# Performance work log

Hardware: AMD Instinct MI355X
Metric: run time of the kernel (lower is better)

## Reference

```python
import jax, jax.numpy as jnp
import numpy as np

N, IN, H, C, E = 50000, 128, 2, 64, 800000
HC = H * C  # 128
NEG_SLOPE = 0.2
EPS_GN = 1e-5


def setup_inputs() -> dict:
    key = jax.random.key(0)
    ks = jax.random.split(key, 32)
    r = lambda i, shape: jax.random.normal(ks[i], shape, dtype=jnp.float32) * 0.1
    inp = {
        'x': jax.random.normal(ks[0], (N, IN), dtype=jnp.float32),
        'edge_index': jax.random.randint(ks[1], (2, E), 0, N, dtype=jnp.int64),
        # conv 0: in=128 -> heads*emb=128
        'Wl0': r(2, (IN, HC)), 'bl0': jnp.zeros((HC,), jnp.float32),
        'Wr0': r(3, (IN, HC)), 'br0': jnp.zeros((HC,), jnp.float32),
        'att0': r(4, (H, C)), 'bias0': jnp.zeros((HC,), jnp.float32),
        # conv 1: in=128 -> 128
        'Wl1': r(5, (HC, HC)), 'bl1': jnp.zeros((HC,), jnp.float32),
        'Wr1': r(6, (HC, HC)), 'br1': jnp.zeros((HC,), jnp.float32),
        'att1': r(7, (H, C)), 'bias1': jnp.zeros((HC,), jnp.float32),
        # GraphNorm params (weight, bias, mean_scale)
        'g0': jnp.ones((HC,), jnp.float32), 'be0': jnp.zeros((HC,), jnp.float32), 'ms0': jnp.ones((HC,), jnp.float32),
        'g1': jnp.ones((HC,), jnp.float32), 'be1': jnp.zeros((HC,), jnp.float32), 'ms1': jnp.ones((HC,), jnp.float32),
        # MLP head
        'W1': r(8, (HC, C)), 'b1': jnp.zeros((C,), jnp.float32),
        'W2': r(9, (C, 2)), 'b2': jnp.zeros((2,), jnp.float32),
    }
    return inp


def gatv2_conv(x, src, dst, Wl, bl, Wr, br, att, bias):
    # PyG GATv2Conv: separate source/target transforms, edge attention, segment softmax
    xl = (x @ Wl + bl).reshape(N, H, C)  # source features
    xr = (x @ Wr + br).reshape(N, H, C)  # target features
    m = jax.nn.leaky_relu(xl[src] + xr[dst], NEG_SLOPE)  # [Etot, H, C]
    e = jnp.einsum('ehc,hc->eh', m, att)                  # [Etot, H]
    emax = jax.ops.segment_max(e, dst, num_segments=N)    # stable softmax per dst
    ex = jnp.exp(e - emax[dst])
    denom = jax.ops.segment_sum(ex, dst, num_segments=N)
    alpha = ex / (denom[dst] + 1e-16)
    out = jax.ops.segment_sum(xl[src] * alpha[:, :, None], dst, num_segments=N)
    return out.reshape(N, HC) + bias


def graph_norm(x, gamma, beta, mean_scale):
    # PyG GraphNorm with batch=None (single graph)
    mean = x.mean(axis=0)
    out = x - mean_scale * mean
    var = (out * out).mean(axis=0)
    return gamma * out / jnp.sqrt(var + EPS_GN) + beta


def reference(x, edge_index, Wl0, bl0, Wr0, br0, att0, bias0,
              Wl1, bl1, Wr1, br1, att1, bias1,
              g0, be0, ms0, g1, be1, ms1, W1, b1, W2, b2):
    loop = jnp.arange(N, dtype=edge_index.dtype)
    src = jnp.concatenate([edge_index[0], loop])  # add_self_loops=True
    dst = jnp.concatenate([edge_index[1], loop])
    # layer 0 (conv + GraphNorm + ReLU)
    h = jax.nn.relu(graph_norm(gatv2_conv(x, src, dst, Wl0, bl0, Wr0, br0, att0, bias0), g0, be0, ms0))
    # layer 1
    h = jax.nn.relu(graph_norm(gatv2_conv(h, src, dst, Wl1, bl1, Wr1, br1, att1, bias1), g1, be1, ms1))
    # dropout is identity in eval mode
    h = jax.nn.relu(h @ W1 + b1)
    return h @ W2 + b2
```

## Files before the change

kernel.cpp:

```cpp
#include <hip/hip_runtime.h>
#include <hip/hip_bf16.h>

#define N_NODES 50000
#define NE      800000
#define NETOT   (NE + N_NODES)
#define NEG     0.2f
#define NBUCK   196
#define NSEG    64
#define SEGCAP  128
#define NCTR    (NBUCK * NSEG)
#define NSLOT   256

typedef unsigned short u16;
typedef unsigned int   u32;
typedef __attribute__((ext_vector_type(8))) short bf16x8;
typedef __attribute__((ext_vector_type(4))) float f32x4;

__device__ __forceinline__ float b2f(u16 v) {
    union { float f; u32 u; } c; c.u = ((u32)v) << 16; return c.f;
}
__device__ __forceinline__ u16 f2b(float f) {
    union { float f; u32 u; } c; c.f = f;
    u32 r = c.u + 0x7FFF + ((c.u >> 16) & 1);
    return (u16)(r >> 16);
}
__device__ __forceinline__ float ldf(const void* p, int i, int fmt) {
    return fmt ? b2f(((const u16*)p)[i]) : ((const float*)p)[i];
}

__device__ __forceinline__ float red16(float p) {
    union { float f; int i; } a, b;
    a.f = p; b.i = __builtin_amdgcn_update_dpp(0, a.i, 0xB1,  0xF, 0xF, true); p += b.f;
    a.f = p; b.i = __builtin_amdgcn_update_dpp(0, a.i, 0x4E,  0xF, 0xF, true); p += b.f;
    a.f = p; b.i = __builtin_amdgcn_update_dpp(0, a.i, 0x141, 0xF, 0xF, true); p += b.f;
    a.f = p; b.i = __builtin_amdgcn_update_dpp(0, a.i, 0x140, 0xF, 0xF, true); p += b.f;
    return p;
}

__device__ __forceinline__ float lrelu(float v) {
    return fmaf(0.4f, fabsf(v), 0.6f * v);
}

__global__ void init_all(const u32* __restrict__ xw, const u32* __restrict__ w0,
                         const int* __restrict__ ei,
                         int* __restrict__ flag, int* __restrict__ bcnt,
                         float* __restrict__ Sp1, float* __restrict__ Sp2) {
    int g = blockIdx.x * 256 + threadIdx.x;
    if (g < NCTR) bcnt[g] = 0;
    for (int i = g; i < NSLOT * 128; i += gridDim.x * 256) {
        Sp1[i] = 0.f; Sp2[i] = 0.f;
    }
    if (blockIdx.x == 0) {
        int wv = threadIdx.x >> 6, l = threadIdx.x & 63;
        if (wv == 0) {
            u32 v = xw[l * 50000 + 1];
            u32 e = (v >> 7) & 0xFF;
            unsigned long long m = __ballot(e >= 100 && e <= 140);
            if (l == 0) { flag[0] = (__popcll(m) >= 48) ? 1 : 0; flag[1] = 0; }
        } else if (wv == 1) {
            u32 v = w0[l * 128 + 1];
            u32 e = (v >> 7) & 0xFF;
            unsigned long long m = __ballot(e >= 100 && e <= 140);
            if (l == 0) flag[3] = (__popcll(m) >= 48) ? 1 : 0;
        } else if (wv == 2) {
            int v = ei[(l * 25000) | 1];
            unsigned long long nz = __ballot(v != 0);
            if (l == 0) flag[2] = (nz == 0ULL) ? 1 : 0;
        }
    }
}

__global__ void bin_a(const int* __restrict__ ei, const int* __restrict__ flag,
                      int* __restrict__ bcnt, u32* __restrict__ pairs) {
    int e = blockIdx.x * 256 + threadIdx.x;
    if (e >= NE) return;
    int f = flag[2];
    int s, d;
    if (f) { s = ei[2 * e]; d = ei[2 * (NE + e)]; }
    else   { s = ei[e];     d = ei[NE + e]; }
    int idx = (d >> 8) * NSEG + (blockIdx.x & (NSEG - 1));
    int pos = atomicAdd(&bcnt[idx], 1);
    if (pos < SEGCAP)
        pairs[(size_t)idx * SEGCAP + pos] = ((u32)(d & 255) << 16) | (u32)s;
}

__global__ __launch_bounds__(256) void bin_b(const u32* __restrict__ pairs,
        const int* __restrict__ bcnt,
        int* __restrict__ indptr, int* __restrict__ srcs) {
    __shared__ int cnt[256];
    __shared__ int scn[256];
    __shared__ int msh[NSEG];
    __shared__ int baseSh;
    int b = blockIdx.x, tid = threadIdx.x;
    int nb0 = b << 8;
    int nodesHere = min(256, N_NODES - nb0);
    if (tid < NSEG) msh[tid] = min(bcnt[b * NSEG + tid], SEGCAP);
    int pre = 0;
    for (int i = tid; i < b * NSEG; i += 256) pre += min(bcnt[i], SEGCAP);
    scn[tid] = pre; __syncthreads();
    for (int off = 128; off > 0; off >>= 1) {
        if (tid < off) scn[tid] += scn[tid + off];
        __syncthreads();
    }
    if (tid == 0) baseSh = scn[0] + nb0;
    __syncthreads();
    int base = baseSh;
    cnt[tid] = (tid < nodesHere) ? 1 : 0;
    __syncthreads();
    const u32* bp = pairs + (size_t)b * NSEG * SEGCAP;
    for (int t = tid; t < NSEG * SEGCAP; t += 256) {
        int seg = t >> 7, i = t & (SEGCAP - 1);
        if (i < msh[seg]) {
            int dloc = (int)(bp[t] >> 16);
            atomicAdd(&cnt[dloc], 1);
        }
    }
    __syncthreads();
    int v = cnt[tid];
    scn[tid] = v; __syncthreads();
    for (int off = 1; off < 256; off <<= 1) {
        int u = (tid >= off) ? scn[tid - off] : 0;
        __syncthreads();
        scn[tid] += u;
        __syncthreads();
    }
    int myoff = base + scn[tid] - v;
    if (tid < nodesHere) indptr[nb0 + tid] = myoff;
    if (tid == 255 && b == NBUCK - 1) indptr[N_NODES] = base + scn[255];
    __syncthreads();
    cnt[tid] = myoff;
    __syncthreads();
    if (tid < nodesHere) {
        int pos = atomicAdd(&cnt[tid], 1);
        srcs[pos] = nb0 + tid;
    }
    for (int t = tid; t < NSEG * SEGCAP; t += 256) {
        int seg = t >> 7, i = t & (SEGCAP - 1);
        if (i < msh[seg]) {
            u32 p = bp[t];
            int pos = atomicAdd(&cnt[p >> 16], 1);
            srcs[pos] = (int)(p & 0xffff);
        }
    }
}

#define LDP 136
#define NT  128
__global__ __launch_bounds__(256) void gemm_xf(const void* __restrict__ inp,
        const int* __restrict__ fin, const int* __restrict__ fw,
        const void* __restrict__ Wl, const void* __restrict__ bl,
        const void* __restrict__ Wr, const void* __restrict__ br,
        const float* __restrict__ nscale, const float* __restrict__ nshift,
        u16* __restrict__ XL, u16* __restrict__ XR) {
    __shared__ u16 As16[NT * LDP];
    __shared__ u16 Bs16[128 * LDP];
    __shared__ float Sc[128], Sh[128];
    int fi = fin[0], fb = fw[0];
    int by = blockIdx.y;
    const void* W  = by ? Wr : Wl;
    const void* bi = by ? br : bl;
    u16* dst       = by ? XR : XL;
    int n0 = blockIdx.x * NT;
    int tid = threadIdx.x;
    bool donorm = (nscale != nullptr);
    if (donorm) {
        if (tid < 128) { Sc[tid] = nscale[tid]; Sh[tid] = nshift[tid]; }
        __syncthreads();
    }
    if (fi) {
        for (int t = tid; t < NT * 16; t += 256) {
            int node = t >> 4, c8 = (t & 15) << 3;
            int n = n0 + node;
            bf16x8 v = {0,0,0,0,0,0,0,0};
            if (n < N_NODES) v = *(const bf16x8*)((const u16*)inp + (size_t)n * 128 + c8);
            *(bf16x8*)&As16[node * LDP + c8] = v;
        }
    } else {
        for (int t = tid; t < NT * 32; t += 256) {
            int node = t >> 5, c4 = (t & 31) << 2;
            int n = n0 + node;
            float4 v = {0.f, 0.f, 0.f, 0.f};
            if (n < N_NODES) v = *(const float4*)((const float*)inp + (size_t)n * 128 + c4);
            if (donorm) {
                v.x = fmaxf(v.x * Sc[c4]     + Sh[c4],     0.f);
                v.y = fmaxf(v.y * Sc[c4 + 1] + Sh[c4 + 1], 0.f);
                v.z = fmaxf(v.z * Sc[c4 + 2] + Sh[c4 + 2], 0.f);
                v.w = fmaxf(v.w * Sc[c4 + 3] + Sh[c4 + 3], 0.f);
            }
            ushort4 h;
            h.x = f2b(v.x); h.y = f2b(v.y); h.z = f2b(v.z); h.w = f2b(v.w);
            *(ushort4*)&As16[node * LDP + c4] = h;
        }
    }
    if (fb) {
        for (int t = tid; t < 128 * 16; t += 256) {
            int k = t >> 4, j8 = (t & 15) << 3;
            bf16x8 v = *(const bf16x8*)((const u16*)W + k * 128 + j8);
            #pragma unroll
            for (int q = 0; q < 8; ++q) Bs16[(j8 + q) * LDP + k] = (u16)v[q];
        }
    } else {
        for (int t = tid; t < 128 * 32; t += 256) {
            int k = t >> 5, j4 = (t & 31) << 2;
            float4 v = *(const float4*)((const float*)W + k * 128 + j4);
            Bs16[(j4 + 0) * LDP + k] = f2b(v.x);
            Bs16[(j4 + 1) * LDP + k] = f2b(v.y);
            Bs16[(j4 + 2) * LDP + k] = f2b(v.z);
            Bs16[(j4 + 3) * LDP + k] = f2b(v.w);
        }
    }
    __syncthreads();

    int wv = tid >> 6, lane = tid & 63;
    int quad = lane >> 4, r = lane & 15;
    int m0 = wv * 32;
    f32x4 acc[2][8];
    #pragma unroll
    for (int mt = 0; mt < 2; ++mt)
        #pragma unroll
        for (int jt = 0; jt < 8; ++jt) acc[mt][jt] = (f32x4){0.f, 0.f, 0.f, 0.f};
    #pragma unroll
    for (int ks = 0; ks < 4; ++ks) {
        int ko = ks * 32 + quad * 8;
        bf16x8 af0 = *(const bf16x8*)&As16[(m0 + r) * LDP + ko];
        bf16x8 af1 = *(const bf16x8*)&As16[(m0 + 16 + r) * LDP + ko];
        #pragma unroll
        for (int jt = 0; jt < 8; ++jt) {
            bf16x8 bfr = *(const bf16x8*)&Bs16[(jt * 16 + r) * LDP + ko];
            acc[0][jt] = __builtin_amdgcn_mfma_f32_16x16x32_bf16(af0, bfr, acc[0][jt], 0, 0, 0);
            acc[1][jt] = __builtin_amdgcn_mfma_f32_16x16x32_bf16(af1, bfr, acc[1][jt], 0, 0, 0);
        }
    }
    __syncthreads();
    #pragma unroll
    for (int jt = 0; jt < 8; ++jt) {
        int j = jt * 16 + r;
        float bj = ldf(bi, j, fb);
        #pragma unroll
        for (int mt = 0; mt < 2; ++mt) {
            #pragma unroll
            for (int reg = 0; reg < 4; ++reg) {
                As16[(m0 + mt * 16 + quad * 4 + reg) * LDP + j] = f2b(acc[mt][jt][reg] + bj);
            }
        }
    }
    __syncthreads();
    #pragma unroll
    for (int rep = 0; rep < 8; ++rep) {
        int idx = rep * 256 + tid;
        int node = idx >> 4, c8 = (idx & 15) << 3;
        int n = n0 + node;
        if (n < N_NODES) {
            bf16x8 v = *(const bf16x8*)&As16[node * LDP + c8];
            *(bf16x8*)(dst + (size_t)n * 128 + c8) = v;
        }
    }
}

__global__ __launch_bounds__(256) void agg_kernel(const u16* __restrict__ XL,
        const u16* __restrict__ XR, const void* __restrict__ att,
        const void* __restrict__ bias,
        const int* __restrict__ fmt,
        const int* __restrict__ indptr, const int* __restrict__ srcs,
        float4* __restrict__ OUT4,
        float* __restrict__ Sp1, float* __restrict__ Sp2) {
    __shared__ float shS1[4 * 128];
    __shared__ float shS2[4 * 128];
    __shared__ int lcount;
    int tid = threadIdx.x;
    int lane = tid & 63;
    int wv = tid >> 6;
    if (tid == 0) lcount = 0;
    __syncthreads();
    int n = blockIdx.x * 4 + wv;
    int eh = lane >> 5, q = lane & 31;
    int fb = fmt[0];
    ushort4 xrv = *(const ushort4*)(XR + (size_t)n * 128 + q * 4);
    float xr0 = b2f(xrv.x), xr1 = b2f(xrv.y), xr2 = b2f(xrv.z), xr3 = b2f(xrv.w);
    float a0 = ldf(att, 4 * q,     fb);
    float a1 = ldf(att, 4 * q + 1, fb);
    float a2 = ldf(att, 4 * q + 2, fb);
    float a3 = ldf(att, 4 * q + 3, fb);
    int beg = indptr[n], end = indptr[n + 1];
    float acc0 = 0.f, acc1 = 0.f, acc2 = 0.f, acc3 = 0.f, dsum = 0.f;
    int nit = (end - beg + 5) / 6;
    for (int it = 0; it < nit; ++it) {
        int iA = beg + 6 * it + eh;
        int iB = iA + 2;
        int iC = iA + 4;
        bool vA = (iA < end), vB = (iB < end), vC = (iC < end);
        int sA = vA ? srcs[iA] : 0;
        int sB = vB ? srcs[iB] : 0;
        int sC = vC ? srcs[iC] : 0;
        ushort4 xa = *(const ushort4*)(XL + (size_t)sA * 128 + q * 4);
        ushort4 xb = *(const ushort4*)(XL + (size_t)sB * 128 + q * 4);
        ushort4 xc = *(const ushort4*)(XL + (size_t)sC * 128 + q * 4);
        float A0 = b2f(xa.x), A1 = b2f(xa.y), A2 = b2f(xa.z), A3 = b2f(xa.w);
        float B0 = b2f(xb.x), B1 = b2f(xb.y), B2v = b2f(xb.z), B3 = b2f(xb.w);
        float C0 = b2f(xc.x), C1 = b2f(xc.y), C2 = b2f(xc.z), C3 = b2f(xc.w);
        float pA = lrelu(A0 + xr0) * a0;
        pA = fmaf(lrelu(A1 + xr1), a1, pA);
        pA = fmaf(lrelu(A2 + xr2), a2, pA);
        pA = fmaf(lrelu(A3 + xr3), a3, pA);
        float pB = lrelu(B0 + xr0) * a0;
        pB = fmaf(lrelu(B1 + xr1), a1, pB);
        pB = fmaf(lrelu(B2v + xr2), a2, pB);
        pB = fmaf(lrelu(B3 + xr3), a3, pB);
        float pC = lrelu(C0 + xr0) * a0;
        pC = fmaf(lrelu(C1 + xr1), a1, pC);
        pC = fmaf(lrelu(C2 + xr2), a2, pC);
        pC = fmaf(lrelu(C3 + xr3), a3, pC);
        pA = red16(pA);
        pB = red16(pB);
        pC = red16(pC);
        float wA = vA ? __expf(fminf(pA, 60.f)) : 0.f;
        float wB = vB ? __expf(fminf(pB, 60.f)) : 0.f;
        float wC = vC ? __expf(fminf(pC, 60.f)) : 0.f;
        acc0 = fmaf(wA, A0, acc0); acc1 = fmaf(wA, A1, acc1);
        acc2 = fmaf(wA, A2, acc2); acc3 = fmaf(wA, A3, acc3);
        acc0 = fmaf(wB, B0, acc0); acc1 = fmaf(wB, B1, acc1);
        acc2 = fmaf(wB, B2v, acc2); acc3 = fmaf(wB, B3, acc3);
        acc0 = fmaf(wC, C0, acc0); acc1 = fmaf(wC, C1, acc1);
        acc2 = fmaf(wC, C2, acc2); acc3 = fmaf(wC, C3, acc3);
        dsum += wA + wB + wC;
    }
    acc0 += __shfl_xor(acc0, 32);
    acc1 += __shfl_xor(acc1, 32);
    acc2 += __shfl_xor(acc2, 32);
    acc3 += __shfl_xor(acc3, 32);
    dsum += __shfl_xor(dsum, 32);
    if (eh == 0) {
        float inv = 1.f / (dsum + 1e-16f);
        float4 o; o.x = acc0 * inv; o.y = acc1 * inv; o.z = acc2 * inv; o.w = acc3 * inv;
        OUT4[(size_t)n * 32 + q] = o;
        float t0 = o.x + ldf(bias, 4 * q,     fb);
        float t1 = o.y + ldf(bias, 4 * q + 1, fb);
        float t2 = o.z + ldf(bias, 4 * q + 2, fb);
        float t3 = o.w + ldf(bias, 4 * q + 3, fb);
        float4 s1; s1.x = t0; s1.y = t1; s1.z = t2; s1.w = t3;
        float4 s2; s2.x = t0 * t0; s2.y = t1 * t1; s2.z = t2 * t2; s2.w = t3 * t3;
        *(float4*)&shS1[wv * 128 + q * 4] = s1;
        *(float4*)&shS2[wv * 128 + q * 4] = s2;
    }
    __threadfence_block();
    int old = 0;
    if (lane == 0) old = atomicAdd(&lcount, 1);
    old = __shfl(old, 0);
    if (old == 3) {
        __threadfence_block();
        int c0 = lane;
        int c1 = lane + 64;
        float s1a = shS1[c0] + shS1[128 + c0] + shS1[256 + c0] + shS1[384 + c0];
        float s1b = shS1[c1] + shS1[128 + c1] + shS1[256 + c1] + shS1[384 + c1];
        float s2a = shS2[c0] + shS2[128 + c0] + shS2[256 + c0] + shS2[384 + c0];
        float s2b = shS2[c1] + shS2[128 + c1] + shS2[256 + c1] + shS2[384 + c1];
        int slot = blockIdx.x & (NSLOT - 1);
        atomicAdd(&Sp1[slot * 128 + c0], s1a);
        atomicAdd(&Sp1[slot * 128 + c1], s1b);
        atomicAdd(&Sp2[slot * 128 + c0], s2a);
        atomicAdd(&Sp2[slot * 128 + c1], s2b);
    }
}

__global__ __launch_bounds__(256) void finalize_norm(float* __restrict__ Sp1,
        float* __restrict__ Sp2,
        const void* __restrict__ gamma, const void* __restrict__ beta,
        const void* __restrict__ msc, const void* __restrict__ bias,
        const int* __restrict__ fmt,
        float* __restrict__ scaleA, float* __restrict__ shiftB) {
    __shared__ float sh1[256], sh2[256];
    int c = blockIdx.x, tid = threadIdx.x;
    sh1[tid] = Sp1[tid * 128 + c];
    sh2[tid] = Sp2[tid * 128 + c];
    Sp1[tid * 128 + c] = 0.f;
    Sp2[tid * 128 + c] = 0.f;
    __syncthreads();
    for (int off = 128; off > 0; off >>= 1) {
        if (tid < off) { sh1[tid] += sh1[tid + off]; sh2[tid] += sh2[tid + off]; }
        __syncthreads();
    }
    if (tid == 0) {
        int fb = fmt[0];
        const float invN = 1.f / (float)N_NODES;
        float mean = sh1[0] * invN;
        float ex2  = sh2[0] * invN;
        float ms = ldf(msc, c, fb);
        float var = ex2 - 2.f * ms * mean * mean + ms * ms * mean * mean;
        float rstd = rsqrtf(var + 1e-5f);
        float A = ldf(gamma, c, fb) * rstd;
        scaleA[c] = A;
        shiftB[c] = ldf(beta, c, fb) - A * (ms * mean - ldf(bias, c, fb));
    }
}

__global__ __launch_bounds__(256) void mlp_kernel(const float* __restrict__ H,
        const void* __restrict__ w1, const void* __restrict__ b1,
        const void* __restrict__ w2, const void* __restrict__ b2,
        const float* __restrict__ nscale, const float* __restrict__ nshift,
        const int* __restrict__ fmt,
        float* __restrict__ out) {
    __shared__ float W1s[128 * 64];
    __shared__ float W2s[128];
    __shared__ float b1s[64];
    __shared__ float Sc[128], Sh[128];
    int tid = threadIdx.x;
    int fb = fmt[0];
    if (fb) {
        for (int t = tid; t < 128 * 8; t += 256) {
            int row8 = t << 3;
            bf16x8 v = *(const bf16x8*)((const u16*)w1 + row8);
            #pragma unroll
            for (int q = 0; q < 8; ++q) W1s[row8 + q] = b2f((u16)v[q]);
        }
    } else {
        for (int t = tid; t < 128 * 64; t += 256) W1s[t] = ((const float*)w1)[t];
    }
    if (tid < 128) { W2s[tid] = ldf(w2, tid, fb); Sc[tid] = nscale[tid]; Sh[tid] = nshift[tid]; }
    if (tid < 64)  b1s[tid] = ldf(b1, tid, fb);
    __syncthreads();
    int n = blockIdx.x * 256 + tid;
    if (n >= N_NODES) return;
    float z[64];
    #pragma unroll
    for (int j = 0; j < 64; j++) z[j] = b1s[j];
    for (int kb = 0; kb < 128; kb += 16) {
        float h[16];
        #pragma unroll
        for (int t = 0; t < 4; t++) {
            float4 v = *(const float4*)&H[n * 128 + kb + t * 4];
            int c = kb + t * 4;
            h[4 * t]     = fmaxf(v.x * Sc[c]     + Sh[c],     0.f);
            h[4 * t + 1] = fmaxf(v.y * Sc[c + 1] + Sh[c + 1], 0.f);
            h[4 * t + 2] = fmaxf(v.z * Sc[c + 2] + Sh[c + 2], 0.f);
            h[4 * t + 3] = fmaxf(v.w * Sc[c + 3] + Sh[c + 3], 0.f);
        }
        #pragma unroll
        for (int i = 0; i < 16; i++) {
            float hv = h[i];
            const float* wrow = &W1s[(kb + i) * 64];
            #pragma unroll
            for (int j = 0; j < 64; j += 4) {
                const float4 w = *(const float4*)&wrow[j];
                z[j]     += hv * w.x;
                z[j + 1] += hv * w.y;
                z[j + 2] += hv * w.z;
                z[j + 3] += hv * w.w;
            }
        }
    }
    float o0 = ldf(b2, 0, fb), o1 = ldf(b2, 1, fb);
    #pragma unroll
    for (int j = 0; j < 64; j++) {
        float zr = fmaxf(z[j], 0.f);
        o0 += zr * W2s[j * 2];
        o1 += zr * W2s[j * 2 + 1];
    }
    if (o0 != o0) o0 = 12345.f;
    if (o1 != o1) o1 = 12345.f;
    float2 o; o.x = o0; o.y = o1;
    ((float2*)out)[n] = o;
}

extern "C" void kernel_launch(void* const* d_in, const int* in_sizes, int n_in,
                              void* d_out, int out_size, void* d_ws, size_t ws_size,
                              hipStream_t stream) {
    (void)in_sizes; (void)n_in; (void)out_size; (void)ws_size;
    const void* x    = d_in[0];
    const int*  ei   = (const int*)d_in[1];
    const void* Wl0  = d_in[2];
    const void* bl0  = d_in[3];
    const void* Wr0  = d_in[4];
    const void* br0  = d_in[5];
    const void* att0 = d_in[6];
    const void* bias0= d_in[7];
    const void* Wl1  = d_in[8];
    const void* bl1  = d_in[9];
    const void* Wr1  = d_in[10];
    const void* br1  = d_in[11];
    const void* att1 = d_in[12];
    const void* bias1= d_in[13];
    const void* g0   = d_in[14];
    const void* be0  = d_in[15];
    const void* ms0  = d_in[16];
    const void* g1   = d_in[17];
    const void* be1  = d_in[18];
    const void* ms1  = d_in[19];
    const void* W1   = d_in[20];
    const void* b1   = d_in[21];
    const void* W2   = d_in[22];
    const void* b2   = d_in[23];

    char* ws = (char*)d_ws;
    const size_t NF2 = (size_t)N_NODES * 128 * 2;
    const size_t NF4 = (size_t)N_NODES * 128 * 4;
    u16*   XLb = (u16*)(ws);
    u16*   XRb = (u16*)(ws + NF2);
    float* B2  = (float*)(ws + 2 * NF2);
    u32*   pairs = (u32*)B2;
    char* small = ws + 2 * NF2 + NF4;
    float* scaleA = (float*)(small + 1024);
    float* shiftB = (float*)(small + 1536);
    int*   flag   = (int*)(small + 2048);
    float* Sp1    = (float*)(small + 4096);
    float* Sp2    = (float*)(small + 4096 + 131072);
    int*   bcnt   = (int*)(small + 4096 + 262144);
    int*   indptr = (int*)(small + 4096 + 262144 + 50176);
    int*   srcs   = indptr + (N_NODES + 64);

    const int* fX   = &flag[0];
    const int* fFP  = &flag[1];
    const int* fPar = &flag[3];

    init_all<<<(NCTR + 255) / 256, 256, 0, stream>>>((const u32*)x, (const u32*)Wl0,
                                                     ei, flag, bcnt, Sp1, Sp2);
    bin_a<<<(NE + 255) / 256, 256, 0, stream>>>(ei, flag, bcnt, pairs);
    bin_b<<<NBUCK, 256, 0, stream>>>(pairs, bcnt, indptr, srcs);

    dim3 ggemm((N_NODES + NT - 1) / NT, 2);

    for (int layer = 0; layer < 2; ++layer) {
        const void* Wl = layer ? Wl1 : Wl0;  const void* bl = layer ? bl1 : bl0;
        const void* Wr = layer ? Wr1 : Wr0;  const void* br = layer ? br1 : br0;
        const void* at = layer ? att1 : att0;
        const void* bi = layer ? bias1 : bias0;
        const void* gm = layer ? g1 : g0;    const void* bt = layer ? be1 : be0;
        const void* mS = layer ? ms1 : ms0;
        const void* inp = layer ? (const void*)B2 : x;
        const int* fin  = layer ? fFP : fX;
        const float* ns = layer ? scaleA : nullptr;
        const float* nh = layer ? shiftB : nullptr;

        gemm_xf<<<ggemm, 256, 0, stream>>>(inp, fin, fPar, Wl, bl, Wr, br, ns, nh,
                                           XLb, XRb);
        agg_kernel<<<(N_NODES + 3) / 4, 256, 0, stream>>>(XLb, XRb, at, bi, fPar,
                                               indptr, srcs, (float4*)B2, Sp1, Sp2);
        finalize_norm<<<128, 256, 0, stream>>>(Sp1, Sp2, gm, bt, mS, bi, fPar,
                                               scaleA, shiftB);
    }

    mlp_kernel<<<(N_NODES + 255) / 256, 256, 0, stream>>>(B2, W1, b1, W2, b2,
                                                          scaleA, shiftB, fPar,
                                                          (float*)d_out);
}
```

Measured before the change: 409.8 us.

## Fuse GraphNorm finalize into aggregation kernel via last-block-done counter

Removes the separate finalize_norm launch per layer. The last aggregation block to finish, detected with a global atomic counter after a threadfence, reduces the per-slot partial sums and writes the norm scale and shift. The slot count drops from 256 to 64 so that final serial reduction stays short. The cost is more atomic contention on fewer slots and a serial tail of work in one wave at the end of the kernel.

```diff
diff --git a/kernel.cpp b/kernel.cpp
--- a/kernel.cpp
+++ b/kernel.cpp
@@ -9,7 +9,8 @@
 #define NSEG    64
 #define SEGCAP  128
 #define NCTR    (NBUCK * NSEG)
-#define NSLOT   256
+#define NSLOT   64
+#define NBLK_AGG ((N_NODES + 3) / 4)
 
 typedef unsigned short u16;
 typedef unsigned int   u32;
@@ -44,12 +45,12 @@
 __global__ void init_all(const u32* __restrict__ xw, const u32* __restrict__ w0,
                          const int* __restrict__ ei,
                          int* __restrict__ flag, int* __restrict__ bcnt,
-                         float* __restrict__ Sp1, float* __restrict__ Sp2) {
+                         float* __restrict__ Sp1, float* __restrict__ Sp2,
+                         int* __restrict__ dctr) {
     int g = blockIdx.x * 256 + threadIdx.x;
     if (g < NCTR) bcnt[g] = 0;
-    for (int i = g; i < NSLOT * 128; i += gridDim.x * 256) {
-        Sp1[i] = 0.f; Sp2[i] = 0.f;
-    }
+    if (g < NSLOT * 128) { Sp1[g] = 0.f; Sp2[g] = 0.f; }
+    if (g == 0) { dctr[0] = 0; dctr[1] = 0; }
     if (blockIdx.x == 0) {
         int wv = threadIdx.x >> 6, l = threadIdx.x & 63;
         if (wv == 0) {
@@ -260,10 +261,14 @@
 __global__ __launch_bounds__(256) void agg_kernel(const u16* __restrict__ XL,
         const u16* __restrict__ XR, const void* __restrict__ att,
         const void* __restrict__ bias,
+        const void* __restrict__ gamma, const void* __restrict__ beta,
+        const void* __restrict__ msc,
         const int* __restrict__ fmt,
         const int* __restrict__ indptr, const int* __restrict__ srcs,
         float4* __restrict__ OUT4,
-        float* __restrict__ Sp1, float* __restrict__ Sp2) {
+        float* __restrict__ Sp1, float* __restrict__ Sp2,
+        float* __restrict__ scaleA, float* __restrict__ shiftB,
+        int* __restrict__ dctr) {
     __shared__ float shS1[4 * 128];
     __shared__ float shS2[4 * 128];
     __shared__ int lcount;
@@ -359,37 +364,34 @@
         atomicAdd(&Sp1[slot * 128 + c1], s1b);
         atomicAdd(&Sp2[slot * 128 + c0], s2a);
         atomicAdd(&Sp2[slot * 128 + c1], s2b);
-    }
-}
-
-__global__ __launch_bounds__(256) void finalize_norm(float* __restrict__ Sp1,
-        float* __restrict__ Sp2,
-        const void* __restrict__ gamma, const void* __restrict__ beta,
-        const void* __restrict__ msc, const void* __restrict__ bias,
-        const int* __restrict__ fmt,
-        float* __restrict__ scaleA, float* __restrict__ shiftB) {
-    __shared__ float sh1[256], sh2[256];
-    int c = blockIdx.x, tid = threadIdx.x;
-    sh1[tid] = Sp1[tid * 128 + c];
-    sh2[tid] = Sp2[tid * 128 + c];
-    Sp1[tid * 128 + c] = 0.f;
-    Sp2[tid * 128 + c] = 0.f;
-    __syncthreads();
-    for (int off = 128; off > 0; off >>= 1) {
-        if (tid < off) { sh1[tid] += sh1[tid + off]; sh2[tid] += sh2[tid + off]; }
-        __syncthreads();
-    }
-    if (tid == 0) {
-        int fb = fmt[0];
-        const float invN = 1.f / (float)N_NODES;
-        float mean = sh1[0] * invN;
-        float ex2  = sh2[0] * invN;
-        float ms = ldf(msc, c, fb);
-        float var = ex2 - 2.f * ms * mean * mean + ms * ms * mean * mean;
-        float rstd = rsqrtf(var + 1e-5f);
-        float A = ldf(gamma, c, fb) * rstd;
-        scaleA[c] = A;
-        shiftB[c] = ldf(beta, c, fb) - A * (ms * mean - ldf(bias, c, fb));
+        __threadfence();
+        int dold = 0;
+        if (lane == 0) dold = atomicAdd(dctr, 1);
+        dold = __shfl(dold, 0);
+        if (dold == NBLK_AGG - 1) {
+            __threadfence();
+            const float invN = 1.f / (float)N_NODES;
+            #pragma unroll
+            for (int h = 0; h < 2; ++h) {
+                int c = lane + h * 64;
+                float s1 = 0.f, s2 = 0.f;
+                for (int s = 0; s < NSLOT; ++s) {
+                    s1 += Sp1[s * 128 + c];
+                    s2 += Sp2[s * 128 + c];
+                    Sp1[s * 128 + c] = 0.f;
+                    Sp2[s * 128 + c] = 0.f;
+                }
+                float mean = s1 * invN;
+                float ex2  = s2 * invN;
+                float ms = ldf(msc, c, fb);
+                float var = ex2 - 2.f * ms * mean * mean + ms * ms * mean * mean;
+                float rstd = rsqrtf(var + 1e-5f);
+                float A = ldf(gamma, c, fb) * rstd;
+                scaleA[c] = A;
+                shiftB[c] = ldf(beta, c, fb) - A * (ms * mean - ldf(bias, c, fb));
+            }
+            if (lane == 0) *dctr = 0;
+        }
     }
 }
 
@@ -501,6 +503,7 @@
     float* scaleA = (float*)(small + 1024);
     float* shiftB = (float*)(small + 1536);
     int*   flag   = (int*)(small + 2048);
+    int*   dctr   = (int*)(small + 3072);
     float* Sp1    = (float*)(small + 4096);
     float* Sp2    = (float*)(small + 4096 + 131072);
     int*   bcnt   = (int*)(small + 4096 + 262144);
@@ -512,7 +515,7 @@
     const int* fPar = &flag[3];
 
     init_all<<<(NCTR + 255) / 256, 256, 0, stream>>>((const u32*)x, (const u32*)Wl0,
-                                                     ei, flag, bcnt, Sp1, Sp2);
+                                                     ei, flag, bcnt, Sp1, Sp2, dctr);
     bin_a<<<(NE + 255) / 256, 256, 0, stream>>>(ei, flag, bcnt, pairs);
     bin_b<<<NBUCK, 256, 0, stream>>>(pairs, bcnt, indptr, srcs);
 
@@ -532,10 +535,9 @@
 
         gemm_xf<<<ggemm, 256, 0, stream>>>(inp, fin, fPar, Wl, bl, Wr, br, ns, nh,
                                            XLb, XRb);
-        agg_kernel<<<(N_NODES + 3) / 4, 256, 0, stream>>>(XLb, XRb, at, bi, fPar,
-                                               indptr, srcs, (float4*)B2, Sp1, Sp2);
-        finalize_norm<<<128, 256, 0, stream>>>(Sp1, Sp2, gm, bt, mS, bi, fPar,
-                                               scaleA, shiftB);
+        agg_kernel<<<NBLK_AGG, 256, 0, stream>>>(XLb, XRb, at, bi, gm, bt, mS, fPar,
+                                               indptr, srcs, (float4*)B2, Sp1, Sp2,
+                                               scaleA, shiftB, &dctr[layer]);
     }
 
     mlp_kernel<<<(N_NODES + 255) / 256, 256, 0, stream>>>(B2, W1, b1, W2, b2,
```

Result: slower. 1.081 ms (+163.7%).
